# Optimization experiments

Measured on AMD Instinct MI355X. Metric: run time of the kernel, lower is better.

The kernel has to match this reference:

```python
import jax, jax.numpy as jnp
import numpy as np

N = 50000   # nodes
E = 800000  # edges (avg degree 16)
D = 128     # in_dim == hidden_dim


def setup_inputs() -> dict:
    key = jax.random.key(0)
    ks = jax.random.split(key, 8)
    x = jax.random.normal(ks[0], (N, D), dtype=jnp.float32)
    edge_index = jax.random.randint(ks[1], (2, E), 0, N, dtype=jnp.int32)
    s = 1.0 / np.sqrt(D)  # glorot-ish scale
    W0 = jax.random.normal(ks[2], (D, D), dtype=jnp.float32) * s
    W1 = jax.random.normal(ks[3], (D, D), dtype=jnp.float32) * s
    W2 = jax.random.normal(ks[4], (D, D), dtype=jnp.float32) * s
    b0 = jnp.zeros((D,), dtype=jnp.float32)
    b1 = jnp.zeros((D,), dtype=jnp.float32)
    b2 = jnp.zeros((D,), dtype=jnp.float32)
    return {"x": x, "edge_index": edge_index,
            "W0": W0, "b0": b0, "W1": W1, "b1": b1, "W2": W2, "b2": b2}


def reference(x, edge_index, W0, b0, W1, b1, W2, b2):
    # PyG GCNConv defaults: add self-loops, symmetric D^-1/2 (A+I) D^-1/2 norm,
    # linear transform first, bias added after aggregation.
    src, dst = edge_index[0], edge_index[1]
    loops = jnp.arange(N, dtype=src.dtype)
    src_f = jnp.concatenate([src, loops])  # [E+N]
    dst_f = jnp.concatenate([dst, loops])
    deg = jax.ops.segment_sum(jnp.ones_like(src_f, dtype=x.dtype), dst_f, num_segments=N)
    dinv = jnp.where(deg > 0, jax.lax.rsqrt(deg), 0.0)
    norm = dinv[src_f] * dinv[dst_f]  # [E+N]

    def gcn_layer(h, W, b):
        h = h @ W                                # [N, D]
        msg = h[src_f] * norm[:, None]           # [E+N, D] gather
        agg = jax.ops.segment_sum(msg, dst_f, num_segments=N)  # scatter-add
        return agg + b

    h = jax.nn.relu(gcn_layer(x, W0, b0))  # dropout p=0.0 is a no-op
    h = jax.nn.relu(gcn_layer(h, W1, b1))
    return gcn_layer(h, W2, b2)
```

## Files before the change

kernel.cpp:

```cpp
#include <hip/hip_runtime.h>
#include <hip/hip_fp16.h>

#define NN 50000
#define NPAD 50048
#define NE 800000
#define D 128
#define BPAD 136

typedef __attribute__((ext_vector_type(8))) short bf16x8;
typedef __attribute__((ext_vector_type(4))) float f32x4;

__device__ inline unsigned short f2bf(float f) {
    unsigned int b = __float_as_uint(f);
    return (unsigned short)((b + 0x7FFFu + ((b >> 16) & 1u)) >> 16);
}
__device__ inline float bf2f(unsigned short u) {
    return __uint_as_float(((unsigned int)u) << 16);
}


__global__ void k_degree(const int* __restrict__ dst, int* __restrict__ cnt) {
    int e = blockIdx.x * 256 + threadIdx.x;
    if (e < NE) atomicAdd(&cnt[dst[e]], 1);
}

__global__ void k_dinv(const int* __restrict__ cnt, float* __restrict__ dinv) {
    int i = blockIdx.x * 256 + threadIdx.x;
    if (i < NN) dinv[i] = rsqrtf((float)(cnt[i] + 1));
}

__global__ void k_scan_block(const int* __restrict__ cnt, int* __restrict__ excl,
                             int* __restrict__ bsum) {
    __shared__ int sm[256];
    int t = threadIdx.x;
    int idx = blockIdx.x * 256 + t;
    int v = (idx < NN) ? cnt[idx] : 0;
    sm[t] = v;
    __syncthreads();
    for (int o = 1; o < 256; o <<= 1) {
        int u = (t >= o) ? sm[t - o] : 0;
        __syncthreads();
        sm[t] += u;
        __syncthreads();
    }
    if (idx < NN) excl[idx] = sm[t] - v;
    if (t == 255) bsum[blockIdx.x] = sm[255];
}

__global__ void k_scan_top(const int* __restrict__ bsum, int* __restrict__ boff) {
    __shared__ int sm[256];
    const int NB = (NN + 255) / 256;
    int t = threadIdx.x;
    int v = (t < NB) ? bsum[t] : 0;
    sm[t] = v;
    __syncthreads();
    for (int o = 1; o < 256; o <<= 1) {
        int u = (t >= o) ? sm[t - o] : 0;
        __syncthreads();
        sm[t] += u;
        __syncthreads();
    }
    if (t < NB) boff[t] = sm[t] - v;
}

__global__ void k_scan_add(int* __restrict__ rowptr, const int* __restrict__ boff) {
    int idx = blockIdx.x * 256 + threadIdx.x;
    if (idx < NN) rowptr[idx] += boff[idx >> 8];
    else if (idx == NN) rowptr[NN] = NE;
}

__global__ void k_fill(const int* __restrict__ src, const int* __restrict__ dst,
                       const int* __restrict__ rowptr, int* __restrict__ fill,
                       int* __restrict__ col) {
    int e = blockIdx.x * 256 + threadIdx.x;
    if (e < NE) {
        int d = dst[e];
        int pos = rowptr[d] + atomicAdd(&fill[d], 1);
        col[pos] = src[e];
    }
}


__global__ void k_convX(const float* __restrict__ X, unsigned short* __restrict__ Xh,
                        unsigned short* __restrict__ Xl) {
    int i4 = blockIdx.x * 256 + threadIdx.x;
    if (i4 >= NN * D / 4) return;
    float4 v = *(const float4*)(X + (size_t)i4 * 4);
    ushort4 h, l;
    h.x = f2bf(v.x); l.x = f2bf(v.x - bf2f(h.x));
    h.y = f2bf(v.y); l.y = f2bf(v.y - bf2f(h.y));
    h.z = f2bf(v.z); l.z = f2bf(v.z - bf2f(h.z));
    h.w = f2bf(v.w); l.w = f2bf(v.w - bf2f(h.w));
    *(ushort4*)(Xh + (size_t)i4 * 4) = h;
    *(ushort4*)(Xl + (size_t)i4 * 4) = l;
}

__global__ void k_convW(const float* __restrict__ W, unsigned short* __restrict__ WhT,
                        unsigned short* __restrict__ WlT) {
    int i = blockIdx.x * 256 + threadIdx.x;
    if (i >= D * D) return;
    int k = i >> 7, c = i & 127;
    float v = W[i];
    unsigned short h = f2bf(v);
    unsigned short l = f2bf(v - bf2f(h));
    WhT[c * D + k] = h;
    WlT[c * D + k] = l;
}


__global__ __launch_bounds__(256, 3) void k_gemm_mfma(
        const unsigned short* __restrict__ Ah, const unsigned short* __restrict__ Al,
        const unsigned short* __restrict__ BhT, const unsigned short* __restrict__ BlT,
        const float* __restrict__ dinv, __half* __restrict__ C) {
    __shared__ short Bs_h[D * BPAD];
    int t = threadIdx.x;
    {
        int c = t >> 1;
        int k0 = (t & 1) * 64;
        const unsigned short* gh = BhT + c * D + k0;
        short* dh = Bs_h + c * BPAD + k0;
        #pragma unroll
        for (int i = 0; i < 8; i++)
            *(int4*)(dh + i * 8) = *(const int4*)(gh + i * 8);
    }
    __syncthreads();

    int w = t >> 6, ln = t & 63;
    int wr = w >> 1, wc = w & 1;
    int R0 = blockIdx.x * 64 + wr * 32;
    int C0 = wc * 64;
    int lr = ln & 15, lg = ln >> 4;

    f32x4 acc[2][4];
    #pragma unroll
    for (int a = 0; a < 2; a++)
        #pragma unroll
        for (int b = 0; b < 4; b++)
            acc[a][b] = (f32x4){0.f, 0.f, 0.f, 0.f};

    const unsigned short* Abh = Ah + (size_t)(R0 + lr) * D + lg * 8;
    const unsigned short* Abl = Al + (size_t)(R0 + lr) * D + lg * 8;

    #pragma unroll
    for (int ks = 0; ks < 4; ks++) {
        int ko = ks * 32;
        bf16x8 fa_h[2], fa_l[2], fb_h[4], fb_l[4];
        #pragma unroll
        for (int fr = 0; fr < 2; fr++) {
            fa_h[fr] = *(const bf16x8*)(Abh + fr * 16 * D + ko);
            fa_l[fr] = *(const bf16x8*)(Abl + fr * 16 * D + ko);
        }
        #pragma unroll
        for (int fc = 0; fc < 4; fc++) {
            int ccol = C0 + fc * 16 + lr;
            fb_h[fc] = *(const bf16x8*)(Bs_h + ccol * BPAD + ko + lg * 8);
            fb_l[fc] = *(const bf16x8*)(BlT + (size_t)ccol * D + ko + lg * 8);
        }
        #pragma unroll
        for (int fr = 0; fr < 2; fr++) {
            #pragma unroll
            for (int fc = 0; fc < 4; fc++) {
                acc[fr][fc] = __builtin_amdgcn_mfma_f32_16x16x32_bf16(
                    fa_h[fr], fb_h[fc], acc[fr][fc], 0, 0, 0);
                acc[fr][fc] = __builtin_amdgcn_mfma_f32_16x16x32_bf16(
                    fa_l[fr], fb_h[fc], acc[fr][fc], 0, 0, 0);
                acc[fr][fc] = __builtin_amdgcn_mfma_f32_16x16x32_bf16(
                    fa_h[fr], fb_l[fc], acc[fr][fc], 0, 0, 0);
            }
        }
    }

    #pragma unroll
    for (int fr = 0; fr < 2; fr++) {
        int rb = R0 + fr * 16 + lg * 4;
        #pragma unroll
        for (int j = 0; j < 4; j++) {
            int r = rb + j;
            if (r < NN) {
                float s = dinv[r];
                #pragma unroll
                for (int fc = 0; fc < 4; fc++)
                    C[(size_t)r * D + C0 + fc * 16 + lr] =
                        __float2half_rn(acc[fr][fc][j] * s);
            }
        }
    }
}


__global__ __launch_bounds__(256) void k_agg(const __half* __restrict__ T,
                                             const int* __restrict__ rowptr,
                                             const int* __restrict__ col,
                                             const float* __restrict__ dinv,
                                             const float* __restrict__ bias,
                                             unsigned short* __restrict__ Oh,
                                             unsigned short* __restrict__ Ol,
                                             float* __restrict__ Of, int mode) {
    int wave = threadIdx.x >> 6;
    int lane = threadIdx.x & 63;
    int i = blockIdx.x * 4 + wave;
    if (i >= NN) return;
    int f = lane * 2;
    float di = dinv[i];
    float2 tv = __half22float2(*(const __half2*)(T + (size_t)i * D + f));
    float ax = tv.x, ay = tv.y;
    int e = rowptr[i], r1 = rowptr[i + 1];
    for (; e + 8 <= r1; e += 8) {
        float2 v[8];
        #pragma unroll
        for (int u = 0; u < 8; u++) {
            int s = col[e + u];
            v[u] = __half22float2(*(const __half2*)(T + (size_t)s * D + f));
        }
        #pragma unroll
        for (int u = 0; u < 8; u++) { ax += v[u].x; ay += v[u].y; }
    }
    for (; e + 4 <= r1; e += 4) {
        float2 v[4];
        #pragma unroll
        for (int u = 0; u < 4; u++) {
            int s = col[e + u];
            v[u] = __half22float2(*(const __half2*)(T + (size_t)s * D + f));
        }
        #pragma unroll
        for (int u = 0; u < 4; u++) { ax += v[u].x; ay += v[u].y; }
    }
    for (; e < r1; e++) {
        int s = col[e];
        float2 sv = __half22float2(*(const __half2*)(T + (size_t)s * D + f));
        ax += sv.x;
        ay += sv.y;
    }
    float2 bv = *(const float2*)(bias + f);
    ax = ax * di + bv.x;
    ay = ay * di + bv.y;
    if (mode) {
        ax = fmaxf(ax, 0.f);
        ay = fmaxf(ay, 0.f);
        unsigned short hx = f2bf(ax), hy = f2bf(ay);
        unsigned short lx = f2bf(ax - bf2f(hx)), ly = f2bf(ay - bf2f(hy));
        *(unsigned int*)(Oh + (size_t)i * D + f) = (unsigned int)hx | ((unsigned int)hy << 16);
        *(unsigned int*)(Ol + (size_t)i * D + f) = (unsigned int)lx | ((unsigned int)ly << 16);
    } else {
        *(float2*)(Of + (size_t)i * D + f) = make_float2(ax, ay);
    }
}


extern "C" void kernel_launch(void* const* d_in, const int* in_sizes, int n_in,
                              void* d_out, int out_size, void* d_ws, size_t ws_size,
                              hipStream_t stream) {
    const float* x  = (const float*)d_in[0];
    const int* edge = (const int*)d_in[1];
    const float* W0 = (const float*)d_in[2];
    const float* b0 = (const float*)d_in[3];
    const float* W1 = (const float*)d_in[4];
    const float* b1 = (const float*)d_in[5];
    const float* W2 = (const float*)d_in[6];
    const float* b2 = (const float*)d_in[7];
    const int* src = edge;
    const int* dst = edge + NE;
    float* out = (float*)d_out;

    char* ws = (char*)d_ws;
    size_t off = 0;
    auto alloc = [&](size_t bytes) {
        void* p = ws + off;
        off += (bytes + 255) & ~(size_t)255;
        return p;
    };
    int*   cnt    = (int*)alloc(NN * 4);
    int*   fill   = (int*)alloc(NN * 4);
    int*   rowptr = (int*)alloc((NN + 1) * 4);
    float* dinv   = (float*)alloc(NN * 4);
    int*   bsum   = (int*)alloc(256 * 4);
    int*   boff   = (int*)alloc(256 * 4);
    int*   col    = (int*)alloc((size_t)NE * 4);
    unsigned short* w0h = (unsigned short*)alloc(D * D * 2);
    unsigned short* w0l = (unsigned short*)alloc(D * D * 2);
    unsigned short* w1h = (unsigned short*)alloc(D * D * 2);
    unsigned short* w1l = (unsigned short*)alloc(D * D * 2);
    unsigned short* w2h = (unsigned short*)alloc(D * D * 2);
    unsigned short* w2l = (unsigned short*)alloc(D * D * 2);
    unsigned short* Xh = (unsigned short*)alloc((size_t)NPAD * D * 2);
    unsigned short* Xl = (unsigned short*)alloc((size_t)NPAD * D * 2);
    __half* T = (__half*)alloc((size_t)NPAD * D * 2);

    hipMemsetAsync(cnt, 0, NN * 4, stream);
    hipMemsetAsync(fill, 0, NN * 4, stream);

    k_degree<<<(NE + 255) / 256, 256, 0, stream>>>(dst, cnt);
    k_dinv<<<(NN + 255) / 256, 256, 0, stream>>>(cnt, dinv);
    k_scan_block<<<(NN + 255) / 256, 256, 0, stream>>>(cnt, rowptr, bsum);
    k_scan_top<<<1, 256, 0, stream>>>(bsum, boff);
    k_scan_add<<<(NN + 256) / 256, 256, 0, stream>>>(rowptr, boff);
    k_fill<<<(NE + 255) / 256, 256, 0, stream>>>(src, dst, rowptr, fill, col);

    k_convW<<<(D * D + 255) / 256, 256, 0, stream>>>(W0, w0h, w0l);
    k_convW<<<(D * D + 255) / 256, 256, 0, stream>>>(W1, w1h, w1l);
    k_convW<<<(D * D + 255) / 256, 256, 0, stream>>>(W2, w2h, w2l);
    k_convX<<<(NN * D / 4 + 255) / 256, 256, 0, stream>>>(x, Xh, Xl);

    const int ggrid = (NN + 63) / 64;
    const int agrid = (NN + 3) / 4;

    k_gemm_mfma<<<ggrid, 256, 0, stream>>>(Xh, Xl, w0h, w0l, dinv, T);
    k_agg<<<agrid, 256, 0, stream>>>(T, rowptr, col, dinv, b0, Xh, Xl, out, 1);
    k_gemm_mfma<<<ggrid, 256, 0, stream>>>(Xh, Xl, w1h, w1l, dinv, T);
    k_agg<<<agrid, 256, 0, stream>>>(T, rowptr, col, dinv, b1, Xh, Xl, out, 1);
    k_gemm_mfma<<<ggrid, 256, 0, stream>>>(Xh, Xl, w2h, w2l, dinv, T);
    k_agg<<<agrid, 256, 0, stream>>>(T, rowptr, col, dinv, b2, Xh, Xl, out, 0);
}
```

Baseline: 282.8 us.

## Fuse X conversion into first GEMM, widen aggregation lanes, trim preprocessing launches

The first layer's GEMM now reads fp32 X directly and splits it into bf16 hi/lo in registers, so the separate X conversion pass and its write/read of two bf16 copies go away. Aggregation switches from one wave per node to half a wave per node, with each lane loading 8 bytes (4 halves), which widens the gather loads. Preprocessing is also trimmed: the edge rank from the degree atomic is reused for CSR fill, removing the second atomic pass and the fill memset. dinv is folded into scan_add and the three weight conversions share one launch. In exchange the fused GEMM drops to 2 blocks per CU and converts A in registers, and aggregation relies on NN being divisible by 8 since its bounds check is gone.

```diff
diff --git a/kernel.cpp b/kernel.cpp
--- a/kernel.cpp
+++ b/kernel.cpp
@@ -19,14 +19,13 @@
 }
 
 
-__global__ void k_degree(const int* __restrict__ dst, int* __restrict__ cnt) {
+__global__ void k_degree(const int* __restrict__ dst, int* __restrict__ cnt,
+                         int* __restrict__ rank) {
     int e = blockIdx.x * 256 + threadIdx.x;
-    if (e < NE) atomicAdd(&cnt[dst[e]], 1);
-}
-
-__global__ void k_dinv(const int* __restrict__ cnt, float* __restrict__ dinv) {
-    int i = blockIdx.x * 256 + threadIdx.x;
-    if (i < NN) dinv[i] = rsqrtf((float)(cnt[i] + 1));
+    if (e < NE) {
+        int d = dst[e];
+        rank[e] = atomicAdd(&cnt[d], 1);
+    }
 }
 
 __global__ void k_scan_block(const int* __restrict__ cnt, int* __restrict__ excl,
@@ -63,50 +62,63 @@
     if (t < NB) boff[t] = sm[t] - v;
 }
 
-__global__ void k_scan_add(int* __restrict__ rowptr, const int* __restrict__ boff) {
+__global__ void k_scan_add(int* __restrict__ rowptr, const int* __restrict__ boff,
+                           const int* __restrict__ cnt, float* __restrict__ dinv) {
     int idx = blockIdx.x * 256 + threadIdx.x;
-    if (idx < NN) rowptr[idx] += boff[idx >> 8];
-    else if (idx == NN) rowptr[NN] = NE;
+    if (idx < NN) {
+        rowptr[idx] += boff[idx >> 8];
+        dinv[idx] = rsqrtf((float)(cnt[idx] + 1));
+    } else if (idx == NN) {
+        rowptr[NN] = NE;
+    }
 }
 
 __global__ void k_fill(const int* __restrict__ src, const int* __restrict__ dst,
-                       const int* __restrict__ rowptr, int* __restrict__ fill,
+                       const int* __restrict__ rowptr, const int* __restrict__ rank,
                        int* __restrict__ col) {
     int e = blockIdx.x * 256 + threadIdx.x;
     if (e < NE) {
         int d = dst[e];
-        int pos = rowptr[d] + atomicAdd(&fill[d], 1);
-        col[pos] = src[e];
-    }
-}
-
-
-__global__ void k_convX(const float* __restrict__ X, unsigned short* __restrict__ Xh,
-                        unsigned short* __restrict__ Xl) {
-    int i4 = blockIdx.x * 256 + threadIdx.x;
-    if (i4 >= NN * D / 4) return;
-    float4 v = *(const float4*)(X + (size_t)i4 * 4);
-    ushort4 h, l;
-    h.x = f2bf(v.x); l.x = f2bf(v.x - bf2f(h.x));
-    h.y = f2bf(v.y); l.y = f2bf(v.y - bf2f(h.y));
-    h.z = f2bf(v.z); l.z = f2bf(v.z - bf2f(h.z));
-    h.w = f2bf(v.w); l.w = f2bf(v.w - bf2f(h.w));
-    *(ushort4*)(Xh + (size_t)i4 * 4) = h;
-    *(ushort4*)(Xl + (size_t)i4 * 4) = l;
-}
-
-__global__ void k_convW(const float* __restrict__ W, unsigned short* __restrict__ WhT,
-                        unsigned short* __restrict__ WlT) {
+        int pos = rowptr[d] + rank[e];
+        __builtin_nontemporal_store(src[e], &col[pos]);
+    }
+}
+
+
+__global__ void k_convW3(const float* __restrict__ W0, const float* __restrict__ W1,
+                         const float* __restrict__ W2, unsigned short* __restrict__ Wh,
+                         unsigned short* __restrict__ Wl) {
     int i = blockIdx.x * 256 + threadIdx.x;
-    if (i >= D * D) return;
-    int k = i >> 7, c = i & 127;
-    float v = W[i];
+    if (i >= 3 * D * D) return;
+    int m = i / (D * D), r = i - m * (D * D);
+    const float* W = (m == 0) ? W0 : ((m == 1) ? W1 : W2);
+    int k = r >> 7, c = r & 127;
+    float v = W[r];
     unsigned short h = f2bf(v);
     unsigned short l = f2bf(v - bf2f(h));
-    WhT[c * D + k] = h;
-    WlT[c * D + k] = l;
-}
-
+    Wh[(size_t)m * D * D + c * D + k] = h;
+    Wl[(size_t)m * D * D + c * D + k] = l;
+}
+
+
+__device__ inline void gemm_store(f32x4 acc[2][4], const float* __restrict__ dinv,
+                                  __half* __restrict__ C, int R0, int C0, int lr, int lg) {
+    #pragma unroll
+    for (int fr = 0; fr < 2; fr++) {
+        int rb = R0 + fr * 16 + lg * 4;
+        #pragma unroll
+        for (int j = 0; j < 4; j++) {
+            int r = rb + j;
+            if (r < NN) {
+                float s = dinv[r];
+                #pragma unroll
+                for (int fc = 0; fc < 4; fc++)
+                    C[(size_t)r * D + C0 + fc * 16 + lr] =
+                        __float2half_rn(acc[fr][fc][j] * s);
+            }
+        }
+    }
+}
 
 __global__ __launch_bounds__(256, 3) void k_gemm_mfma(
         const unsigned short* __restrict__ Ah, const unsigned short* __restrict__ Al,
@@ -169,22 +181,77 @@
             }
         }
     }
-
-    #pragma unroll
-    for (int fr = 0; fr < 2; fr++) {
-        int rb = R0 + fr * 16 + lg * 4;
-        #pragma unroll
-        for (int j = 0; j < 4; j++) {
-            int r = rb + j;
-            if (r < NN) {
-                float s = dinv[r];
-                #pragma unroll
-                for (int fc = 0; fc < 4; fc++)
-                    C[(size_t)r * D + C0 + fc * 16 + lr] =
-                        __float2half_rn(acc[fr][fc][j] * s);
+    gemm_store(acc, dinv, C, R0, C0, lr, lg);
+}
+
+__global__ __launch_bounds__(256, 2) void k_gemm_mfma_x(
+        const float* __restrict__ X,
+        const unsigned short* __restrict__ BhT, const unsigned short* __restrict__ BlT,
+        const float* __restrict__ dinv, __half* __restrict__ C) {
+    __shared__ short Bs_h[D * BPAD];
+    int t = threadIdx.x;
+    {
+        int c = t >> 1;
+        int k0 = (t & 1) * 64;
+        const unsigned short* gh = BhT + c * D + k0;
+        short* dh = Bs_h + c * BPAD + k0;
+        #pragma unroll
+        for (int i = 0; i < 8; i++)
+            *(int4*)(dh + i * 8) = *(const int4*)(gh + i * 8);
+    }
+    __syncthreads();
+
+    int w = t >> 6, ln = t & 63;
+    int wr = w >> 1, wc = w & 1;
+    int R0 = blockIdx.x * 64 + wr * 32;
+    int C0 = wc * 64;
+    int lr = ln & 15, lg = ln >> 4;
+
+    f32x4 acc[2][4];
+    #pragma unroll
+    for (int a = 0; a < 2; a++)
+        #pragma unroll
+        for (int b = 0; b < 4; b++)
+            acc[a][b] = (f32x4){0.f, 0.f, 0.f, 0.f};
+
+    const float* Ab = X + (size_t)(R0 + lr) * D + lg * 8;
+
+    #pragma unroll
+    for (int ks = 0; ks < 4; ks++) {
+        int ko = ks * 32;
+        bf16x8 fa_h[2], fa_l[2], fb_h[4], fb_l[4];
+        #pragma unroll
+        for (int fr = 0; fr < 2; fr++) {
+            float4 p0 = *(const float4*)(Ab + fr * 16 * D + ko);
+            float4 p1 = *(const float4*)(Ab + fr * 16 * D + ko + 4);
+            float vv[8] = {p0.x, p0.y, p0.z, p0.w, p1.x, p1.y, p1.z, p1.w};
+            #pragma unroll
+            for (int j = 0; j < 8; j++) {
+                unsigned short h = f2bf(vv[j]);
+                fa_h[fr][j] = (short)h;
+                fa_l[fr][j] = (short)f2bf(vv[j] - bf2f(h));
             }
         }
-    }
+        #pragma unroll
+        for (int fc = 0; fc < 4; fc++) {
+            int ccol = C0 + fc * 16 + lr;
+            fb_h[fc] = *(const bf16x8*)(Bs_h + ccol * BPAD + ko + lg * 8);
+            fb_l[fc] = *(const bf16x8*)(BlT + (size_t)ccol * D + ko + lg * 8);
+        }
+        #pragma unroll
+        for (int fr = 0; fr < 2; fr++) {
+            #pragma unroll
+            for (int fc = 0; fc < 4; fc++) {
+                acc[fr][fc] = __builtin_amdgcn_mfma_f32_16x16x32_bf16(
+                    fa_h[fr], fb_h[fc], acc[fr][fc], 0, 0, 0);
+                acc[fr][fc] = __builtin_amdgcn_mfma_f32_16x16x32_bf16(
+                    fa_l[fr], fb_h[fc], acc[fr][fc], 0, 0, 0);
+                acc[fr][fc] = __builtin_amdgcn_mfma_f32_16x16x32_bf16(
+                    fa_h[fr], fb_l[fc], acc[fr][fc], 0, 0, 0);
+            }
+        }
+    }
+    gemm_store(acc, dinv, C, R0, C0, lr, lg);
 }
 
 
@@ -196,53 +263,71 @@
                                              unsigned short* __restrict__ Oh,
                                              unsigned short* __restrict__ Ol,
                                              float* __restrict__ Of, int mode) {
-    int wave = threadIdx.x >> 6;
-    int lane = threadIdx.x & 63;
-    int i = blockIdx.x * 4 + wave;
-    if (i >= NN) return;
-    int f = lane * 2;
+    int i = blockIdx.x * 8 + (threadIdx.x >> 5);
+    int sl = threadIdx.x & 31;
+    int f = sl * 4;
     float di = dinv[i];
-    float2 tv = __half22float2(*(const __half2*)(T + (size_t)i * D + f));
-    float ax = tv.x, ay = tv.y;
+    float2 raw = *(const float2*)(T + (size_t)i * D + f);
+    __half2 s0 = *(__half2*)&raw.x, s1 = *(__half2*)&raw.y;
+    float2 g0 = __half22float2(s0), g1 = __half22float2(s1);
+    float a0 = g0.x, a1 = g0.y, a2 = g1.x, a3 = g1.y;
+
     int e = rowptr[i], r1 = rowptr[i + 1];
     for (; e + 8 <= r1; e += 8) {
-        float2 v[8];
+        float2 rv[8];
         #pragma unroll
         for (int u = 0; u < 8; u++) {
             int s = col[e + u];
-            v[u] = __half22float2(*(const __half2*)(T + (size_t)s * D + f));
-        }
-        #pragma unroll
-        for (int u = 0; u < 8; u++) { ax += v[u].x; ay += v[u].y; }
+            rv[u] = *(const float2*)(T + (size_t)s * D + f);
+        }
+        #pragma unroll
+        for (int u = 0; u < 8; u++) {
+            __half2 x0 = *(__half2*)&rv[u].x, x1 = *(__half2*)&rv[u].y;
+            float2 q0 = __half22float2(x0), q1 = __half22float2(x1);
+            a0 += q0.x; a1 += q0.y; a2 += q1.x; a3 += q1.y;
+        }
     }
     for (; e + 4 <= r1; e += 4) {
-        float2 v[4];
+        float2 rv[4];
         #pragma unroll
         for (int u = 0; u < 4; u++) {
             int s = col[e + u];
-            v[u] = __half22float2(*(const __half2*)(T + (size_t)s * D + f));
-        }
-        #pragma unroll
-        for (int u = 0; u < 4; u++) { ax += v[u].x; ay += v[u].y; }
+            rv[u] = *(const float2*)(T + (size_t)s * D + f);
+        }
+        #pragma unroll
+        for (int u = 0; u < 4; u++) {
+            __half2 x0 = *(__half2*)&rv[u].x, x1 = *(__half2*)&rv[u].y;
+            float2 q0 = __half22float2(x0), q1 = __half22float2(x1);
+            a0 += q0.x; a1 += q0.y; a2 += q1.x; a3 += q1.y;
+        }
     }
     for (; e < r1; e++) {
         int s = col[e];
-        float2 sv = __half22float2(*(const __half2*)(T + (size_t)s * D + f));
-        ax += sv.x;
-        ay += sv.y;
-    }
-    float2 bv = *(const float2*)(bias + f);
-    ax = ax * di + bv.x;
-    ay = ay * di + bv.y;
+        float2 rv = *(const float2*)(T + (size_t)s * D + f);
+        __half2 x0 = *(__half2*)&rv.x, x1 = *(__half2*)&rv.y;
+        float2 q0 = __half22float2(x0), q1 = __half22float2(x1);
+        a0 += q0.x; a1 += q0.y; a2 += q1.x; a3 += q1.y;
+    }
+
+    float4 bv = *(const float4*)(bias + f);
+    a0 = a0 * di + bv.x;
+    a1 = a1 * di + bv.y;
+    a2 = a2 * di + bv.z;
+    a3 = a3 * di + bv.w;
     if (mode) {
-        ax = fmaxf(ax, 0.f);
-        ay = fmaxf(ay, 0.f);
-        unsigned short hx = f2bf(ax), hy = f2bf(ay);
-        unsigned short lx = f2bf(ax - bf2f(hx)), ly = f2bf(ay - bf2f(hy));
-        *(unsigned int*)(Oh + (size_t)i * D + f) = (unsigned int)hx | ((unsigned int)hy << 16);
-        *(unsigned int*)(Ol + (size_t)i * D + f) = (unsigned int)lx | ((unsigned int)ly << 16);
+        a0 = fmaxf(a0, 0.f); a1 = fmaxf(a1, 0.f);
+        a2 = fmaxf(a2, 0.f); a3 = fmaxf(a3, 0.f);
+        unsigned short h0 = f2bf(a0), h1 = f2bf(a1), h2 = f2bf(a2), h3 = f2bf(a3);
+        unsigned short l0 = f2bf(a0 - bf2f(h0)), l1 = f2bf(a1 - bf2f(h1));
+        unsigned short l2 = f2bf(a2 - bf2f(h2)), l3 = f2bf(a3 - bf2f(h3));
+        uint2 ph = make_uint2((unsigned)h0 | ((unsigned)h1 << 16),
+                              (unsigned)h2 | ((unsigned)h3 << 16));
+        uint2 pl = make_uint2((unsigned)l0 | ((unsigned)l1 << 16),
+                              (unsigned)l2 | ((unsigned)l3 << 16));
+        *(uint2*)(Oh + (size_t)i * D + f) = ph;
+        *(uint2*)(Ol + (size_t)i * D + f) = pl;
     } else {
-        *(float2*)(Of + (size_t)i * D + f) = make_float2(ax, ay);
+        *(float4*)(Of + (size_t)i * D + f) = make_float4(a0, a1, a2, a3);
     }
 }
 
@@ -270,44 +355,34 @@
         return p;
     };
     int*   cnt    = (int*)alloc(NN * 4);
-    int*   fill   = (int*)alloc(NN * 4);
     int*   rowptr = (int*)alloc((NN + 1) * 4);
     float* dinv   = (float*)alloc(NN * 4);
     int*   bsum   = (int*)alloc(256 * 4);
     int*   boff   = (int*)alloc(256 * 4);
+    int*   rank   = (int*)alloc((size_t)NE * 4);
     int*   col    = (int*)alloc((size_t)NE * 4);
-    unsigned short* w0h = (unsigned short*)alloc(D * D * 2);
-    unsigned short* w0l = (unsigned short*)alloc(D * D * 2);
-    unsigned short* w1h = (unsigned short*)alloc(D * D * 2);
-    unsigned short* w1l = (unsigned short*)alloc(D * D * 2);
-    unsigned short* w2h = (unsigned short*)alloc(D * D * 2);
-    unsigned short* w2l = (unsigned short*)alloc(D * D * 2);
+    unsigned short* Wh = (unsigned short*)alloc(3 * D * D * 2);
+    unsigned short* Wl = (unsigned short*)alloc(3 * D * D * 2);
     unsigned short* Xh = (unsigned short*)alloc((size_t)NPAD * D * 2);
     unsigned short* Xl = (unsigned short*)alloc((size_t)NPAD * D * 2);
     __half* T = (__half*)alloc((size_t)NPAD * D * 2);
 
     hipMemsetAsync(cnt, 0, NN * 4, stream);
-    hipMemsetAsync(fill, 0, NN * 4, stream);
-
-    k_degree<<<(NE + 255) / 256, 256, 0, stream>>>(dst, cnt);
-    k_dinv<<<(NN + 255) / 256, 256, 0, stream>>>(cnt, dinv);
+
+    k_degree<<<(NE + 255) / 256, 256, 0, stream>>>(dst, cnt, rank);
     k_scan_block<<<(NN + 255) / 256, 256, 0, stream>>>(cnt, rowptr, bsum);
     k_scan_top<<<1, 256, 0, stream>>>(bsum, boff);
-    k_scan_add<<<(NN + 256) / 256, 256, 0, stream>>>(rowptr, boff);
-    k_fill<<<(NE + 255) / 256, 256, 0, stream>>>(src, dst, rowptr, fill, col);
-
-    k_convW<<<(D * D + 255) / 256, 256, 0, stream>>>(W0, w0h, w0l);
-    k_convW<<<(D * D + 255) / 256, 256, 0, stream>>>(W1, w1h, w1l);
-    k_convW<<<(D * D + 255) / 256, 256, 0, stream>>>(W2, w2h, w2l);
-    k_convX<<<(NN * D / 4 + 255) / 256, 256, 0, stream>>>(x, Xh, Xl);
+    k_scan_add<<<(NN + 256) / 256, 256, 0, stream>>>(rowptr, boff, cnt, dinv);
+    k_fill<<<(NE + 255) / 256, 256, 0, stream>>>(src, dst, rowptr, rank, col);
+    k_convW3<<<(3 * D * D + 255) / 256, 256, 0, stream>>>(W0, W1, W2, Wh, Wl);
 
     const int ggrid = (NN + 63) / 64;
-    const int agrid = (NN + 3) / 4;
-
-    k_gemm_mfma<<<ggrid, 256, 0, stream>>>(Xh, Xl, w0h, w0l, dinv, T);
+    const int agrid = NN / 8;
+
+    k_gemm_mfma_x<<<ggrid, 256, 0, stream>>>(x, Wh, Wl, dinv, T);
     k_agg<<<agrid, 256, 0, stream>>>(T, rowptr, col, dinv, b0, Xh, Xl, out, 1);
-    k_gemm_mfma<<<ggrid, 256, 0, stream>>>(Xh, Xl, w1h, w1l, dinv, T);
+    k_gemm_mfma<<<ggrid, 256, 0, stream>>>(Xh, Xl, Wh + D * D, Wl + D * D, dinv, T);
     k_agg<<<agrid, 256, 0, stream>>>(T, rowptr, col, dinv, b1, Xh, Xl, out, 1);
-    k_gemm_mfma<<<ggrid, 256, 0, stream>>>(Xh, Xl, w2h, w2l, dinv, T);
+    k_gemm_mfma<<<ggrid, 256, 0, stream>>>(Xh, Xl, Wh + 2 * D * D, Wl + 2 * D * D, dinv, T);
     k_agg<<<agrid, 256, 0, stream>>>(T, rowptr, col, dinv, b2, Xh, Xl, out, 0);
 }
```

New measurement: 244.0 us. -13.7%, faster.
